# Kernel optimization log

Hardware: AMD Instinct MI355X
Metric: run time of the kernel (lower is better)

## Reference

```python
import jax, jax.numpy as jnp
import numpy as np

B, S, D, H, SPAN = 4, 1024, 768, 12, 512
HD = D // H  # 64


def setup_inputs() -> dict:
    key = jax.random.key(0)
    ks = jax.random.split(key, 8)
    hidden_states = jax.random.normal(ks[0], (B, S, D), jnp.float32)
    rel_embeddings = jax.random.normal(ks[1], (2 * SPAN, D), jnp.float32) * 0.02
    Wq = jax.random.normal(ks[2], (D, D), jnp.float32) * 0.02
    Wk = jax.random.normal(ks[3], (D, D), jnp.float32) * 0.02
    Wv = jax.random.normal(ks[4], (D, D), jnp.float32) * 0.02
    Wo = jax.random.normal(ks[5], (D, D), jnp.float32) * 0.02
    bq = jnp.zeros((D,), jnp.float32); bk = jnp.zeros((D,), jnp.float32)
    bv = jnp.zeros((D,), jnp.float32); bo = jnp.zeros((D,), jnp.float32)
    ln_g = jnp.ones((D,), jnp.float32); ln_b = jnp.zeros((D,), jnp.float32)
    idx = jnp.arange(S)
    relative_pos = (idx[:, None] - idx[None, :]).astype(jnp.int32)  # q - k
    lengths = jnp.array([1024, 896, 768, 512])  # padding-style mask
    valid = idx[None, :] < lengths[:, None]  # [B,S]
    attention_mask = (valid[:, :, None] & valid[:, None, :])[:, None, :, :].astype(jnp.int32)  # [B,1,S,S]
    return dict(hidden_states=hidden_states, rel_embeddings=rel_embeddings,
                Wq=Wq, bq=bq, Wk=Wk, bk=bk, Wv=Wv, bv=bv, Wo=Wo, bo=bo,
                ln_g=ln_g, ln_b=ln_b, attention_mask=attention_mask,
                relative_pos=relative_pos)


def reference(hidden_states, rel_embeddings, Wq, bq, Wk, bk, Wv, bv, Wo, bo,
              ln_g, ln_b, attention_mask, relative_pos):
    # content projections -> [B,H,S,HD]
    q = (hidden_states @ Wq.T + bq).reshape(B, S, H, HD).transpose(0, 2, 1, 3)
    k = (hidden_states @ Wk.T + bk).reshape(B, S, H, HD).transpose(0, 2, 1, 3)
    v = (hidden_states @ Wv.T + bv).reshape(B, S, H, HD).transpose(0, 2, 1, 3)

    scale_qk = jnp.sqrt(jnp.float32(HD * 3))  # scale_factor = 3
    scores = jnp.einsum('bhqd,bhkd->bhqk', q, k) / scale_qk

    # shared-key position projections -> [H, 2*SPAN, HD]
    pos_q = (rel_embeddings @ Wq.T + bq).reshape(2 * SPAN, H, HD).transpose(1, 0, 2)
    pos_k = (rel_embeddings @ Wk.T + bk).reshape(2 * SPAN, H, HD).transpose(1, 0, 2)

    rp = relative_pos.astype(jnp.int32)
    # c2p: query vs relative key-position embedding, gathered by clamp(rel+span)
    c2p_att = jnp.einsum('bhqd,hkd->bhqk', q, pos_k)  # [B,H,S,2*SPAN]
    c2p_pos = jnp.clip(rp + SPAN, 0, 2 * SPAN - 1)
    c2p_idx = jnp.broadcast_to(c2p_pos[None, None], (B, H, S, S))
    c2p = jnp.take_along_axis(c2p_att, c2p_idx, axis=-1) / scale_qk

    # p2c: key vs relative query-position embedding, gathered by clamp(-rel+span), then transposed
    p2c_att = jnp.einsum('bhkd,hqd->bhkq', k, pos_q)  # [B,H,S,2*SPAN]
    p2c_pos = jnp.clip(SPAN - rp, 0, 2 * SPAN - 1)
    p2c_idx = jnp.broadcast_to(p2c_pos[None, None], (B, H, S, S))
    p2c = jnp.swapaxes(jnp.take_along_axis(p2c_att, p2c_idx, axis=-1), -1, -2)
    p2c = p2c / jnp.sqrt(jnp.float32(HD))  # note: torch uses sqrt(d) here, no scale_factor

    scores = scores + c2p + p2c

    # XSoftmax: masked softmax with zeros at masked positions
    mask = attention_mask.astype(bool)  # [B,1,S,S]
    neg = jnp.finfo(scores.dtype).min
    probs = jax.nn.softmax(jnp.where(mask, scores, neg), axis=-1)
    probs = jnp.where(mask, probs, jnp.float32(0))

    ctx = jnp.einsum('bhqk,bhkd->bhqd', probs, v).transpose(0, 2, 1, 3).reshape(B, S, D)

    # DebertaV2SelfOutput: dense + residual + LayerNorm(eps=1e-7)
    x = ctx @ Wo.T + bo + hidden_states
    mu = x.mean(-1, keepdims=True)
    var = ((x - mu) ** 2).mean(-1, keepdims=True)
    return (x - mu) / jnp.sqrt(var + 1e-7) * ln_g + ln_b
```

## Files before the change

### kernel.cpp

```cpp
#include <hip/hip_runtime.h>
#include <hip/hip_bf16.h>
#include <stdint.h>

typedef __hip_bfloat16 bf16;
typedef __attribute__((ext_vector_type(8))) short s8v;
typedef __attribute__((ext_vector_type(4))) float f4v;

__device__ __align__(16) bf16 g_hidden[4096 * 768];
__device__ __align__(16) bf16 g_rel[1024 * 768];
__device__ __align__(16) bf16 g_Wqkv[2304 * 768];
__device__ __align__(16) bf16 g_Wo[768 * 768];
__device__ __align__(16) bf16 g_biasQKV[2304];
__device__ __align__(16) bf16 g_biasPos[1536];
__device__ __align__(16) bf16 g_bo[768];
__device__ __align__(16) bf16 g_lng[768];
__device__ __align__(16) bf16 g_lnb[768];
__device__ __align__(16) bf16 g_Y1[4096 * 1536];
__device__ __align__(16) bf16 g_VT[48u * 64 * 1024];
__device__ __align__(16) bf16 g_Yp[1024 * 1536];
__device__ __align__(16) bf16 g_C2P[48u * 1024 * 1024];
__device__ __align__(16) bf16 g_P2Cd[48u * 1024 * 1024];
__device__ __align__(16) bf16 g_p2cL[48 * 1024];
__device__ __align__(16) bf16 g_p2cR[48 * 1024];
__device__ __align__(16) bf16 g_ctx[4096 * 768];
__device__ __align__(16) float g_X[4096 * 768];
__device__ int g_vq[4096], g_vk[4096], g_kmax[4];

__device__ __forceinline__ float bfs(short x) {
  return __uint_as_float(((unsigned int)(unsigned short)x) << 16);
}
__device__ __forceinline__ unsigned short f2bf(float f) {
  bf16 h = __float2bfloat16(f);
  return *(unsigned short*)&h;
}
__device__ __forceinline__ bool detect_bf16(const void* lng_raw) {
  return *(const unsigned int*)lng_raw == 0x3F803F80u;
}

__device__ __forceinline__ void cvt4(const void* src, bf16* dst, long grp, bool isbf) {
  long e = grp * 4;
  if (isbf) {
    *(uint2*)(dst + e) = *(const uint2*)((const bf16*)src + e);
  } else {
    float4 f = *(const float4*)((const float*)src + e);
    union { unsigned short us[4]; uint2 v; } u;
    u.us[0] = f2bf(f.x); u.us[1] = f2bf(f.y); u.us[2] = f2bf(f.z); u.us[3] = f2bf(f.w);
    *(uint2*)(dst + e) = u.v;
  }
}

__global__ __launch_bounds__(256) void cvt_inputs(
    const void* h, const void* r,
    const void* wq, const void* wk, const void* wv, const void* wo,
    const void* bq, const void* bk, const void* bv, const void* bo,
    const void* lg, const void* lb)
{
  if (blockIdx.x == 0 && threadIdx.x < 4) g_kmax[threadIdx.x] = 0;
  const bool isbf = detect_bf16(lg);
  long i = (long)blockIdx.x * 256 + threadIdx.x;
  if (i < 786432) { cvt4(h,  g_hidden,          i, isbf); return; } i -= 786432;
  if (i < 196608) { cvt4(r,  g_rel,             i, isbf); return; } i -= 196608;
  if (i < 147456) { cvt4(wq, g_Wqkv,            i, isbf); return; } i -= 147456;
  if (i < 147456) { cvt4(wk, g_Wqkv + 589824,   i, isbf); return; } i -= 147456;
  if (i < 147456) { cvt4(wv, g_Wqkv + 1179648,  i, isbf); return; } i -= 147456;
  if (i < 147456) { cvt4(wo, g_Wo,              i, isbf); return; } i -= 147456;
  if (i < 192)    { cvt4(bq, g_biasQKV,         i, isbf); return; } i -= 192;
  if (i < 192)    { cvt4(bk, g_biasQKV + 768,   i, isbf); return; } i -= 192;
  if (i < 192)    { cvt4(bv, g_biasQKV + 1536,  i, isbf); return; } i -= 192;
  if (i < 192)    { cvt4(bq, g_biasPos,         i, isbf); return; } i -= 192;
  if (i < 192)    { cvt4(bk, g_biasPos + 768,   i, isbf); return; } i -= 192;
  if (i < 192)    { cvt4(lg, g_lng,             i, isbf); return; } i -= 192;
  if (i < 192)    { cvt4(lb, g_lnb,             i, isbf); return; }
}

__global__ __launch_bounds__(256) void mask_prep(const int* __restrict__ mask) {
  int t = blockIdx.x * 256 + threadIdx.x;
  int b = t >> 10, i = t & 1023;
  int vq = mask[((size_t)(b * 1024 + i)) * 1024];
  int vk = mask[((size_t)(b * 1024)) * 1024 + i];
  g_vq[t] = vq;
  g_vk[t] = vk;
  if (vq | vk) atomicMax(&g_kmax[b], i + 1);
}

__global__ __launch_bounds__(256, 2) void gemm_bt(int which) {
  __shared__ short As[128][72];
  __shared__ short Bs[128][72];

  const bf16 *A, *B; const bf16* bias;
  int lda, ldb, K, mode;
  const int m0 = blockIdx.y * 128, n0 = blockIdx.x * 128;

  if (which == 0) {
    A = g_hidden; lda = 768; B = g_Wqkv; ldb = 768; bias = g_biasQKV; K = 768;
    mode = (n0 >= 1536) ? 5 : 0;
  } else if (which == 1) {
    A = g_rel; lda = 768; B = g_Wqkv; ldb = 768; bias = g_biasPos; K = 768; mode = 1;
  } else {
    A = g_ctx; lda = 768; B = g_Wo; ldb = 768; bias = g_bo; K = 768; mode = 4;
  }

  const int tid = threadIdx.x, wave = tid >> 6, lane = tid & 63;
  const int quad = lane >> 4, l15 = lane & 15;
  const int wm = (wave >> 1) * 64, wn = (wave & 1) * 64;
  const int sr = tid >> 2, sc8 = (tid & 3) * 16;

  f4v acc[4][4];
#pragma unroll
  for (int i = 0; i < 4; i++)
#pragma unroll
    for (int j = 0; j < 4; j++) acc[i][j] = (f4v){0.f, 0.f, 0.f, 0.f};

  uint4 pa0, pa1, pa2, pa3, pb0, pb1, pb2, pb3;
#define LOAD_T(k0)                                                           \
  {                                                                          \
    const bf16* ap = A + (size_t)(m0 + sr) * lda + (k0) + sc8;               \
    const bf16* ap2 = A + (size_t)(m0 + sr + 64) * lda + (k0) + sc8;         \
    const bf16* bp = B + (size_t)(n0 + sr) * ldb + (k0) + sc8;               \
    const bf16* bp2 = B + (size_t)(n0 + sr + 64) * ldb + (k0) + sc8;         \
    pa0 = *(const uint4*)ap;  pa1 = *(const uint4*)(ap + 8);                 \
    pa2 = *(const uint4*)ap2; pa3 = *(const uint4*)(ap2 + 8);                \
    pb0 = *(const uint4*)bp;  pb1 = *(const uint4*)(bp + 8);                 \
    pb2 = *(const uint4*)bp2; pb3 = *(const uint4*)(bp2 + 8);                \
  }

  LOAD_T(0)
  for (int k0 = 0; k0 < K; k0 += 64) {
    __syncthreads();
    *(uint4*)&As[sr][sc8] = pa0;      *(uint4*)&As[sr][sc8 + 8] = pa1;
    *(uint4*)&As[sr + 64][sc8] = pa2; *(uint4*)&As[sr + 64][sc8 + 8] = pa3;
    *(uint4*)&Bs[sr][sc8] = pb0;      *(uint4*)&Bs[sr][sc8 + 8] = pb1;
    *(uint4*)&Bs[sr + 64][sc8] = pb2; *(uint4*)&Bs[sr + 64][sc8 + 8] = pb3;
    __syncthreads();
    if (k0 + 64 < K) LOAD_T(k0 + 64)

    s8v af[4][2], bfr[4][2];
#pragma unroll
    for (int mt = 0; mt < 4; mt++) {
      af[mt][0] = *(const s8v*)&As[wm + mt * 16 + l15][quad * 8];
      af[mt][1] = *(const s8v*)&As[wm + mt * 16 + l15][32 + quad * 8];
    }
#pragma unroll
    for (int nt = 0; nt < 4; nt++) {
      bfr[nt][0] = *(const s8v*)&Bs[wn + nt * 16 + l15][quad * 8];
      bfr[nt][1] = *(const s8v*)&Bs[wn + nt * 16 + l15][32 + quad * 8];
    }
#pragma unroll
    for (int mt = 0; mt < 4; mt++)
#pragma unroll
      for (int nt = 0; nt < 4; nt++) {
        acc[mt][nt] = __builtin_amdgcn_mfma_f32_16x16x32_bf16(af[mt][0], bfr[nt][0], acc[mt][nt], 0, 0, 0);
        acc[mt][nt] = __builtin_amdgcn_mfma_f32_16x16x32_bf16(af[mt][1], bfr[nt][1], acc[mt][nt], 0, 0, 0);
      }
  }
#undef LOAD_T

  float biasv[4];
#pragma unroll
  for (int nt = 0; nt < 4; nt++)
    biasv[nt] = bfs(*(const short*)&bias[n0 + wn + nt * 16 + l15]);

#pragma unroll
  for (int mt = 0; mt < 4; mt++) {
#pragma unroll
    for (int nt = 0; nt < 4; nt++) {
      const int mbase = m0 + wm + mt * 16 + quad * 4;
      const int n = n0 + wn + nt * 16 + l15;
      if (mode == 5) {
        const int dd = n - 1536, hv = dd >> 6, hd = dd & 63;
        const int bb = mbase >> 10, ss = mbase & 1023;
        float t0 = acc[mt][nt][0] + biasv[nt], t1 = acc[mt][nt][1] + biasv[nt];
        float t2 = acc[mt][nt][2] + biasv[nt], t3 = acc[mt][nt][3] + biasv[nt];
        uint2 pk;
        pk.x = (unsigned int)f2bf(t0) | ((unsigned int)f2bf(t1) << 16);
        pk.y = (unsigned int)f2bf(t2) | ((unsigned int)f2bf(t3) << 16);
        *(uint2*)(g_VT + (((size_t)(bb * 12 + hv) * 64 + hd) << 10) + ss) = pk;
        continue;
      }
#pragma unroll
      for (int reg = 0; reg < 4; reg++) {
        const int m = mbase + reg;
        float v = acc[mt][nt][reg] + biasv[nt];
        if (mode == 0) {
          g_Y1[(size_t)m * 1536 + n] = __float2bfloat16(v);
        } else if (mode == 1) {
          g_Yp[(size_t)m * 1536 + n] = __float2bfloat16(v);
        } else {
          v += bfs(*(const short*)&g_hidden[(size_t)m * 768 + n]);
          g_X[(size_t)m * 768 + n] = v;
        }
      }
    }
  }
}

__global__ __launch_bounds__(256, 2) void band_gemm() {
  const int z = blockIdx.z;
  const int which = z / 48, bh = z % 48;
  const int b = bh / 12, hh = bh - b * 12;
  const int m0 = blockIdx.y * 128, n0 = blockIdx.x * 128;
  const int kmax = g_kmax[b];
  if (m0 >= kmax) return;
  const int lo = max(0, m0 + 513 - kmax);
  const int hi = min(1023, m0 + 639);
  if (n0 + 127 < lo || n0 > hi) return;

  const bf16* A = g_Y1 + (size_t)(b * 1024) * 1536 + (which ? 768 : 0) + hh * 64;
  const bf16* Bp = g_Yp + (which ? 0 : 768) + hh * 64;

  __shared__ short As[128][68], Bs[128][68];
  __shared__ short S[128][132];
  const int tid = threadIdx.x, wave = tid >> 6, lane = tid & 63;
  const int quad = lane >> 4, l15 = lane & 15;
  const int wm = (wave >> 1) * 64, wn = (wave & 1) * 64;
  const int sr = tid >> 2, sc = (tid & 3) * 16;

  {
    const bf16* a0 = A + (size_t)(m0 + sr) * 1536 + sc;
    const bf16* a1 = A + (size_t)(m0 + sr + 64) * 1536 + sc;
    const bf16* b0 = Bp + (size_t)(n0 + sr) * 1536 + sc;
    const bf16* b1 = Bp + (size_t)(n0 + sr + 64) * 1536 + sc;
    *(uint4*)&As[sr][sc]          = *(const uint4*)a0;
    *(uint4*)&As[sr][sc + 8]      = *(const uint4*)(a0 + 8);
    *(uint4*)&As[sr + 64][sc]     = *(const uint4*)a1;
    *(uint4*)&As[sr + 64][sc + 8] = *(const uint4*)(a1 + 8);
    *(uint4*)&Bs[sr][sc]          = *(const uint4*)b0;
    *(uint4*)&Bs[sr][sc + 8]      = *(const uint4*)(b0 + 8);
    *(uint4*)&Bs[sr + 64][sc]     = *(const uint4*)b1;
    *(uint4*)&Bs[sr + 64][sc + 8] = *(const uint4*)(b1 + 8);
  }
  __syncthreads();

  s8v af[4][2], bfr[4][2];
#pragma unroll
  for (int mt = 0; mt < 4; mt++) {
    af[mt][0] = *(const s8v*)&As[wm + mt * 16 + l15][quad * 8];
    af[mt][1] = *(const s8v*)&As[wm + mt * 16 + l15][32 + quad * 8];
  }
#pragma unroll
  for (int nt = 0; nt < 4; nt++) {
    bfr[nt][0] = *(const s8v*)&Bs[wn + nt * 16 + l15][quad * 8];
    bfr[nt][1] = *(const s8v*)&Bs[wn + nt * 16 + l15][32 + quad * 8];
  }

  f4v acc[4][4];
#pragma unroll
  for (int mt = 0; mt < 4; mt++)
#pragma unroll
    for (int nt = 0; nt < 4; nt++) {
      acc[mt][nt] = __builtin_amdgcn_mfma_f32_16x16x32_bf16(af[mt][0], bfr[nt][0], (f4v){0.f, 0.f, 0.f, 0.f}, 0, 0, 0);
      acc[mt][nt] = __builtin_amdgcn_mfma_f32_16x16x32_bf16(af[mt][1], bfr[nt][1], acc[mt][nt], 0, 0, 0);
    }

  if (which == 0) {
    bf16* Cp = g_C2P + ((size_t)bh << 20);
#pragma unroll
    for (int mt = 0; mt < 4; mt++)
#pragma unroll
      for (int nt = 0; nt < 4; nt++) {
        const int m = m0 + wm + mt * 16 + quad * 4;
        const int n = n0 + wn + nt * 16 + l15;
#pragma unroll
        for (int reg = 0; reg < 4; reg++)
          Cp[(size_t)(m + reg) * 1024 + n] = __float2bfloat16(acc[mt][nt][reg]);
      }
    return;
  }

#pragma unroll
  for (int mt = 0; mt < 4; mt++)
#pragma unroll
    for (int nt = 0; nt < 4; nt++)
#pragma unroll
      for (int reg = 0; reg < 4; reg++)
        S[wm + mt * 16 + quad * 4 + reg][wn + nt * 16 + l15] =
            (short)f2bf(acc[mt][nt][reg]);
  __syncthreads();

  if (n0 == 0 && tid < 128)
    g_p2cL[bh * 1024 + m0 + tid] = *(bf16*)&S[tid][0];
  if (n0 == 896 && tid < 128)
    g_p2cR[bh * 1024 + m0 + tid] = *(bf16*)&S[tid][127];

  bf16* Pd = g_P2Cd + ((size_t)bh << 20);
  for (int s = wave; s < 255; s += 4) {
    const int dl = s - 127;
    const int r = (n0 - m0) + dl + 511;
    if (r < 0 || r > 1023) continue;
    const int mlo = max(0, -dl), mhi = min(127, 127 - dl);
    bf16* dst = Pd + ((size_t)r << 10) + m0;
    for (int i = mlo + lane; i <= mhi; i += 64)
      dst[i] = *(bf16*)&S[i][i + dl];
  }
}

__global__ __launch_bounds__(256, 4) void attn_mfma() {
  const int bh = blockIdx.y, b = bh / 12, hh = bh - b * 12;
  const int q0 = blockIdx.x * 64;
  const int tid = threadIdx.x, wave = tid >> 6, lane = tid & 63;
  const int quad = lane >> 4, l15 = lane & 15;
  const int kmax = g_kmax[b];

  if (q0 >= kmax) {
    uint4 zz = {0u, 0u, 0u, 0u};
#pragma unroll
    for (int s = tid; s < 512; s += 256) {
      int r = s >> 3, cc = (s & 7) * 8;
      *(uint4*)(g_ctx + (size_t)(b * 1024 + q0 + r) * 768 + hh * 64 + cc) = zz;
    }
    return;
  }

  __shared__ short Ks[64][68], VTs[64][68], Pl[4][16][68];

  const size_t qrow = (size_t)(b * 1024 + q0 + wave * 16 + l15) * 1536 + hh * 64;
  const s8v qf0 = *(const s8v*)(g_Y1 + qrow + quad * 8);
  const s8v qf1 = *(const s8v*)(g_Y1 + qrow + 32 + quad * 8);

  int vqr[4];
#pragma unroll
  for (int reg = 0; reg < 4; reg++)
    vqr[reg] = g_vq[b * 1024 + q0 + wave * 16 + quad * 4 + reg];

  f4v accO[4];
#pragma unroll
  for (int dt = 0; dt < 4; dt++) accO[dt] = (f4v){0.f, 0.f, 0.f, 0.f};
  float psum[4] = {0.f, 0.f, 0.f, 0.f};

  const int sr = tid >> 2, sc8 = (tid & 3) * 16;
  const bf16* Kbase = g_Y1 + (size_t)(b * 1024) * 1536 + 768 + hh * 64;
  const bf16* Vbase = g_VT + ((size_t)bh << 16);
  const bf16* __restrict__ C2Pb = g_C2P + ((size_t)bh << 20);
  const bf16* __restrict__ P2Cdb = g_P2Cd + ((size_t)bh << 20);
  const bf16* __restrict__ p2cLb = g_p2cL + bh * 1024;
  const bf16* __restrict__ p2cRb = g_p2cR + bh * 1024;
  const int qg = q0 + wave * 16 + quad * 4;

  uint4 rk0, rk1, rv0, rv1;
#define LOAD_A(k0)                                                         \
  {                                                                        \
    const bf16* kp = Kbase + (size_t)((k0) + sr) * 1536 + sc8;             \
    rk0 = *(const uint4*)kp; rk1 = *(const uint4*)(kp + 8);                \
    const bf16* vp = Vbase + ((size_t)sr << 10) + (k0) + sc8;              \
    rv0 = *(const uint4*)vp; rv1 = *(const uint4*)(vp + 8);                \
  }

  LOAD_A(0)
  const float r192 = 0.0721687836487032f;
  const float r64 = 0.125f;

  for (int k0 = 0; k0 < kmax; k0 += 64) {
    __syncthreads();
    *(uint4*)&Ks[sr][sc8] = rk0;   *(uint4*)&Ks[sr][sc8 + 8] = rk1;
    *(uint4*)&VTs[sr][sc8] = rv0;  *(uint4*)&VTs[sr][sc8 + 8] = rv1;

    short c2s[16], p2i[16], plv[4], prv[4];
#pragma unroll
    for (int nt = 0; nt < 4; nt++) {
      const int k = k0 + nt * 16 + l15;
      plv[nt] = *(const short*)(p2cLb + k);
      prv[nt] = *(const short*)(p2cRb + k);
#pragma unroll
      for (int reg = 0; reg < 4; reg++) {
        const int q = qg + reg;
        const int cc = min(max(q - k + 512, 0), 1023);
        c2s[nt * 4 + reg] = *(const short*)(C2Pb + (((size_t)q) << 10) + cc);
        p2i[nt * 4 + reg] = *(const short*)(P2Cdb + (((size_t)(1023 - q)) << 10) + k);
      }
    }

    if (k0 + 64 < kmax) LOAD_A(k0 + 64)
    __syncthreads();

    f4v sacc[4];
#pragma unroll
    for (int nt = 0; nt < 4; nt++) {
      s8v kb0 = *(const s8v*)&Ks[nt * 16 + l15][quad * 8];
      s8v kb1 = *(const s8v*)&Ks[nt * 16 + l15][32 + quad * 8];
      sacc[nt] = __builtin_amdgcn_mfma_f32_16x16x32_bf16(qf0, kb0, (f4v){0.f, 0.f, 0.f, 0.f}, 0, 0, 0);
      sacc[nt] = __builtin_amdgcn_mfma_f32_16x16x32_bf16(qf1, kb1, sacc[nt], 0, 0, 0);
    }

    const bool tail = (k0 + 64 > kmax);
#pragma unroll
    for (int nt = 0; nt < 4; nt++) {
      const int kl = nt * 16 + l15;
#pragma unroll
      for (int reg = 0; reg < 4; reg++) {
        const int q = qg + reg;
        const int d2 = (k0 + kl) - q + 512;
        short p2s = (d2 < 0) ? plv[nt] : ((d2 > 1023) ? prv[nt] : p2i[nt * 4 + reg]);
        float c2 = bfs(c2s[nt * 4 + reg]);
        float sc = (sacc[nt][reg] + c2) * r192 + bfs(p2s) * r64;
        float pe = __expf(fminf(sc, 60.f));
        if (tail && (k0 + kl >= kmax)) pe = 0.f;
        psum[reg] += pe;
        Pl[wave][quad * 4 + reg][kl] = (short)f2bf(pe);
      }
    }

    s8v pa0 = *(const s8v*)&Pl[wave][l15][quad * 8];
    s8v pa1 = *(const s8v*)&Pl[wave][l15][32 + quad * 8];
#pragma unroll
    for (int dt = 0; dt < 4; dt++) {
      s8v vb0 = *(const s8v*)&VTs[dt * 16 + l15][quad * 8];
      s8v vb1 = *(const s8v*)&VTs[dt * 16 + l15][32 + quad * 8];
      accO[dt] = __builtin_amdgcn_mfma_f32_16x16x32_bf16(pa0, vb0, accO[dt], 0, 0, 0);
      accO[dt] = __builtin_amdgcn_mfma_f32_16x16x32_bf16(pa1, vb1, accO[dt], 0, 0, 0);
    }
  }
#undef LOAD_A

#pragma unroll
  for (int off = 1; off < 16; off <<= 1)
#pragma unroll
    for (int reg = 0; reg < 4; reg++) psum[reg] += __shfl_xor(psum[reg], off);

  float inv[4];
#pragma unroll
  for (int reg = 0; reg < 4; reg++)
    inv[reg] = (vqr[reg] != 0 && psum[reg] > 0.f) ? 1.f / psum[reg] : 0.f;

#pragma unroll
  for (int dt = 0; dt < 4; dt++)
#pragma unroll
    for (int reg = 0; reg < 4; reg++) {
      float v = accO[dt][reg] * inv[reg];
      g_ctx[(size_t)(b * 1024 + q0 + wave * 16 + quad * 4 + reg) * 768 + hh * 64 + dt * 16 + l15] =
          __float2bfloat16(v);
    }
}

__global__ __launch_bounds__(256) void ln_kernel(const void* lng_raw, void* out) {
  const bool isbf = detect_bf16(lng_raw);
  const int row = blockIdx.x;
  const int tid = threadIdx.x;
  const float* xr = g_X + (size_t)row * 768;
  float x0 = xr[tid], x1 = xr[tid + 256], x2 = xr[tid + 512];
  float s = x0 + x1 + x2;
  float s2 = x0 * x0 + x1 * x1 + x2 * x2;
#pragma unroll
  for (int off = 32; off; off >>= 1) { s += __shfl_xor(s, off); s2 += __shfl_xor(s2, off); }
  __shared__ float red[2][4];
  int w = tid >> 6, ln = tid & 63;
  if (ln == 0) { red[0][w] = s; red[1][w] = s2; }
  __syncthreads();
  float ts = red[0][0] + red[0][1] + red[0][2] + red[0][3];
  float ts2 = red[1][0] + red[1][1] + red[1][2] + red[1][3];
  float mu = ts * (1.f / 768.f);
  float var = fmaxf(ts2 * (1.f / 768.f) - mu * mu, 0.f);
  float rstd = rsqrtf(var + 1e-7f);
#pragma unroll
  for (int q = 0; q < 3; q++) {
    int cidx = tid + q * 256;
    float xv = (q == 0) ? x0 : (q == 1 ? x1 : x2);
    float gg = bfs(*(const short*)&g_lng[cidx]);
    float bb = bfs(*(const short*)&g_lnb[cidx]);
    float val = (xv - mu) * rstd * gg + bb;
    if (isbf) ((bf16*)out)[(size_t)row * 768 + cidx] = __float2bfloat16(val);
    else      ((float*)out)[(size_t)row * 768 + cidx] = val;
  }
}

extern "C" void kernel_launch(void* const* d_in, const int* in_sizes, int n_in,
                              void* d_out, int out_size, void* d_ws, size_t ws_size,
                              hipStream_t stream) {
  const int* amask = (const int*)d_in[12];
  (void)d_ws; (void)ws_size; (void)in_sizes; (void)n_in; (void)out_size;

  cvt_inputs<<<dim3(6150), 256, 0, stream>>>(
      d_in[0], d_in[1], d_in[2], d_in[4], d_in[6], d_in[8],
      d_in[3], d_in[5], d_in[7], d_in[9], d_in[10], d_in[11]);
  mask_prep<<<dim3(16), 256, 0, stream>>>(amask);
  gemm_bt<<<dim3(18, 32, 1), 256, 0, stream>>>(0);
  gemm_bt<<<dim3(12, 8, 1), 256, 0, stream>>>(1);
  band_gemm<<<dim3(8, 8, 96), 256, 0, stream>>>();
  attn_mfma<<<dim3(16, 48), 256, 0, stream>>>();
  gemm_bt<<<dim3(6, 32, 1), 256, 0, stream>>>(4);
  ln_kernel<<<dim3(4096), 256, 0, stream>>>(d_in[10], d_out);
}
```

Baseline: 428.0 us.

## Alias band_gemm LDS buffers and vectorize diagonal P2C stores

The band_gemm kernel's A/B staging tiles and the score scratch tile now share one LDS allocation. A barrier is added before the scores overwrite the staging data. This cuts shared memory per block, which can let more blocks fit per CU. The diagonal scatter into P2Cd now writes 8 bf16 values per lane as 16-byte stores, with scalar handling for the unaligned head or tail, instead of one 2-byte store per lane.

Result: no change. 426.2 us (-0.4%).

```diff
diff --git a/kernel.cpp b/kernel.cpp
--- a/kernel.cpp
+++ b/kernel.cpp
@@ -208,8 +208,12 @@
   const bf16* A = g_Y1 + (size_t)(b * 1024) * 1536 + (which ? 768 : 0) + hh * 64;
   const bf16* Bp = g_Yp + (which ? 0 : 768) + hh * 64;
 
-  __shared__ short As[128][68], Bs[128][68];
-  __shared__ short S[128][132];
+  __shared__ short SH[2][128][72];
+  short (*As)[72] = SH[0];
+  short (*Bs)[72] = SH[1];
+  short* Sb = &SH[0][0][0];
+#define SS(i, j) Sb[(i) * 136 + (j)]
+
   const int tid = threadIdx.x, wave = tid >> 6, lane = tid & 63;
   const int quad = lane >> 4, l15 = lane & 15;
   const int wm = (wave >> 1) * 64, wn = (wave & 1) * 64;
@@ -267,20 +271,21 @@
     return;
   }
 
+  __syncthreads();
 #pragma unroll
   for (int mt = 0; mt < 4; mt++)
 #pragma unroll
     for (int nt = 0; nt < 4; nt++)
 #pragma unroll
       for (int reg = 0; reg < 4; reg++)
-        S[wm + mt * 16 + quad * 4 + reg][wn + nt * 16 + l15] =
+        SS(wm + mt * 16 + quad * 4 + reg, wn + nt * 16 + l15) =
             (short)f2bf(acc[mt][nt][reg]);
   __syncthreads();
 
   if (n0 == 0 && tid < 128)
-    g_p2cL[bh * 1024 + m0 + tid] = *(bf16*)&S[tid][0];
+    g_p2cL[bh * 1024 + m0 + tid] = *(bf16*)&SS(tid, 0);
   if (n0 == 896 && tid < 128)
-    g_p2cR[bh * 1024 + m0 + tid] = *(bf16*)&S[tid][127];
+    g_p2cR[bh * 1024 + m0 + tid] = *(bf16*)&SS(tid, 127);
 
   bf16* Pd = g_P2Cd + ((size_t)bh << 20);
   for (int s = wave; s < 255; s += 4) {
@@ -289,9 +294,28 @@
     if (r < 0 || r > 1023) continue;
     const int mlo = max(0, -dl), mhi = min(127, 127 - dl);
     bf16* dst = Pd + ((size_t)r << 10) + m0;
-    for (int i = mlo + lane; i <= mhi; i += 64)
-      dst[i] = *(bf16*)&S[i][i + dl];
-  }
+    const int v0 = (mlo + 7) & ~7;
+    const int v1 = (mhi + 1) & ~7;
+    for (int i8 = v0 + lane * 8; i8 < v1; i8 += 512) {
+      union { unsigned short us[8]; uint4 q; } u;
+#pragma unroll
+      for (int t = 0; t < 8; t++)
+        u.us[t] = (unsigned short)SS(i8 + t, i8 + t + dl);
+      *(uint4*)(dst + i8) = u.q;
+    }
+    if (dl < 0) {
+      if (lane < v0 - mlo) {
+        const int i = mlo + lane;
+        dst[i] = *(bf16*)&SS(i, i + dl);
+      }
+    } else {
+      if (lane < mhi + 1 - v1) {
+        const int i = v1 + lane;
+        dst[i] = *(bf16*)&SS(i, i + dl);
+      }
+    }
+  }
+#undef SS
 }
 
 __global__ __launch_bounds__(256, 4) void attn_mfma() {
```
